# Kernel optimization log

Measured on AMD Instinct MI355X. Metric: run time of the kernel, lower is better.

The kernel has to match this reference:

```python
import jax, jax.numpy as jnp
import numpy as np

# Model hyperparameters (match init_kwargs)
G = 256      # graph_size
K = 6        # conv kernel size
CH = 8       # channels
ROWS = 4
COLS = 3
B = 64       # batch
H = G - K + 1  # conv output side (square) = 251


def setup_inputs() -> dict:
    key = jax.random.key(0)
    k1, k2, k3, k4 = jax.random.split(key, 4)
    x = jax.random.normal(k1, (B, G, G), dtype=jnp.float32)
    # Conv2d(1, CH, (K,K)) weights, kaiming_normal_ (fan_in = 1*K*K, gain=sqrt(2))
    fan_in = 1 * K * K
    conv_w = jax.random.normal(k2, (CH, 1, K, K), dtype=jnp.float32) * np.float32(np.sqrt(2.0 / fan_in))
    # torch Conv2d default bias init: U(-1/sqrt(fan_in), 1/sqrt(fan_in))
    bound = np.float32(1.0 / np.sqrt(fan_in))
    conv_b = jax.random.uniform(k3, (CH,), dtype=jnp.float32, minval=-bound, maxval=bound)
    # coef parameter [CH, ROWS, COLS], kaiming_normal_ (fan_in = ROWS*COLS)
    coef = jax.random.normal(k4, (CH, ROWS, COLS), dtype=jnp.float32) * np.float32(np.sqrt(2.0 / (ROWS * COLS)))
    return {"x": x, "conv_w": conv_w, "conv_b": conv_b, "coef": coef}


def _traces_of_powers(C):
    """C: [H,H]. Returns traces of C^(i+2) for i in 0..ROWS-1 (matches torch loop:
    x_series[0]=C@C; at step i it records trace(x_series[i]) = trace(C^(i+2))."""
    def step(P, _):
        return C @ P, jnp.trace(P)
    _, ts = jax.lax.scan(step, C @ C, None, length=ROWS)
    return ts  # [ROWS]


def reference(x, conv_w, conv_b, coef):
    # conv over each sample treated as [1,1,G,G] -> vectorized as [B,1,G,G]
    y = jax.lax.conv_general_dilated(
        x[:, None], conv_w, window_strides=(1, 1), padding='VALID',
        dimension_numbers=('NCHW', 'OIHW', 'NCHW'))
    y = y + conv_b[None, :, None, None]           # [B, CH, H, H]

    ts = jax.vmap(jax.vmap(_traces_of_powers))(y)  # [B, CH, ROWS]

    jpow = jnp.arange(1, COLS + 1, dtype=jnp.float32)            # exponents j+1
    ret = ts[..., None] ** jpow                                  # [B, CH, ROWS, COLS]
    numel = jnp.float32(H * H)
    exps = (jnp.arange(ROWS, dtype=jnp.float32)[:, None]
            + jnp.arange(COLS, dtype=jnp.float32)[None, :] + 1.0)  # i+j+1
    ret = ret / (numel ** exps)                                  # [B, CH, ROWS, COLS]

    terms = coef[None] * ret
    return terms.sum(axis=(1, 2, 3))  # [B]
```

## Files before the change

### kernel.cpp

```cpp
#include <hip/hip_runtime.h>

typedef short short8 __attribute__((ext_vector_type(8)));
typedef float f32x4 __attribute__((ext_vector_type(4)));

#define B_    64
#define CH_   8
#define NBC   512
#define MATU  65536
#define H_    251
#define PADX  76
#define LDSW  40

#define SEL_HI 0x07060302u
#define SEL_LO 0x05040100u

__device__ inline unsigned short bf16r(float f){
    unsigned u = __float_as_uint(f);
    u += 0x7fffu + ((u >> 16) & 1u);
    return (unsigned short)(u >> 16);
}
__device__ inline float bf16f(unsigned short h){ return __uint_as_float(((unsigned)h) << 16); }
__device__ inline unsigned packsplit(float v){
    unsigned short h = bf16r(v);
    unsigned short l = bf16r(v - bf16f(h));
    return (((unsigned)h) << 16) | (unsigned)l;
}
__device__ inline float unpackf(unsigned u){
    return __uint_as_float(u & 0xffff0000u) + bf16f((unsigned short)(u & 0xffffu));
}

__global__ __launch_bounds__(256) void conv_pack(const float* __restrict__ x,
                                                 const float* __restrict__ w,
                                                 const float* __restrict__ bias,
                                                 unsigned* __restrict__ Ypk,
                                                 int b_base) {
    __shared__ float xt[69 * PADX];
    __shared__ float wsm[148];

    int tid = threadIdx.x;
    int tile = blockIdx.x;
    int lb = blockIdx.y;
    int cq = blockIdx.z;
    int b = b_base + lb;
    int r0 = (tile >> 2) * 64, c0 = (tile & 3) * 64;

    if (tid < 144) wsm[tid] = w[cq * 144 + tid];
    if (tid < 4)   wsm[144 + tid] = bias[cq * 4 + tid];

    const float* xb = x + (size_t)b * 65536;
    for (int idx = tid; idx < 69 * 19; idx += 256) {
        int row = idx / 19, chq = idx - row * 19;
        int gr = r0 + row, gc = c0 + chq * 4;
        float4 v = make_float4(0.f, 0.f, 0.f, 0.f);
        if (gr < 256 && gc < 256) v = *(const float4*)(xb + gr * 256 + gc);
        *(float4*)&xt[row * PADX + chq * 4] = v;
    }
    __syncthreads();

    int tx = tid & 15, ty = tid >> 4;

    float acc[4][4][4];
    #pragma unroll
    for (int cc = 0; cc < 4; ++cc) {
        float bv = wsm[144 + cc];
        #pragma unroll
        for (int i = 0; i < 4; ++i)
            #pragma unroll
            for (int j = 0; j < 4; ++j) acc[cc][i][j] = bv;
    }

    #pragma unroll
    for (int ir = 0; ir < 9; ++ir) {
        float row[9];
        {
            const float* xr = &xt[(ty * 4 + ir) * PADX + tx * 4];
            float4 ra = *(const float4*)xr;
            float4 rb = *(const float4*)(xr + 4);
            row[0] = ra.x; row[1] = ra.y; row[2] = ra.z; row[3] = ra.w;
            row[4] = rb.x; row[5] = rb.y; row[6] = rb.z; row[7] = rb.w;
            row[8] = xr[8];
        }
        #pragma unroll
        for (int cc = 0; cc < 4; ++cc) {
            const float* wc = &wsm[cc * 36];
            #pragma unroll
            for (int i = 0; i < 4; ++i) {
                int u = ir - i;
                if (u >= 0 && u < 6) {
                    #pragma unroll
                    for (int v = 0; v < 6; ++v) {
                        float wv = wc[u * 6 + v];
                        #pragma unroll
                        for (int j = 0; j < 4; ++j) acc[cc][i][j] += row[j + v] * wv;
                    }
                }
            }
        }
    }

    #pragma unroll
    for (int cc = 0; cc < 4; ++cc) {
        int ch = cq * 4 + cc;
        unsigned pk[4][4];
        #pragma unroll
        for (int i = 0; i < 4; ++i) {
            int gr = r0 + ty * 4 + i;
            #pragma unroll
            for (int j = 0; j < 4; ++j) {
                int gc = c0 + tx * 4 + j;
                float v = (gr < H_ && gc < H_) ? acc[cc][i][j] : 0.f;
                pk[i][j] = packsplit(v);
            }
        }
        unsigned* yrow = Ypk + (size_t)(lb * 8 + ch) * MATU;
        #pragma unroll
        for (int i = 0; i < 4; ++i) {
            uint4 v = make_uint4(pk[i][0], pk[i][1], pk[i][2], pk[i][3]);
            *(uint4*)&yrow[(size_t)(r0 + ty * 4 + i) * 256 + c0 + tx * 4] = v;
        }
    }
}

template<int PHASE>
__global__ __launch_bounds__(256, 4) void gemm_mfma(const unsigned* __restrict__ Apk,
                                                    const unsigned* __restrict__ Ypk,
                                                    unsigned* __restrict__ Mpk,
                                                    double* __restrict__ pdiag,
                                                    double* __restrict__ pfull,
                                                    int bc_base, int cur) {
    __shared__ __align__(16) char smem[36864];
    __shared__ double redbuf[8];

    unsigned short* Ahi = (unsigned short*)smem;
    unsigned short* Alo = (unsigned short*)(smem + 10240);
    unsigned short* Bhi = (unsigned short*)(smem + 20480);
    unsigned short* Blo = (unsigned short*)(smem + 28672);

    int tid = threadIdx.x;

    int hw = blockIdx.x;
    int xcd = hw & 7, s = hw >> 3;
    int mpx = cur >> 3;
    int lbc = xcd * mpx + (s >> 2);
    int t4 = s & 3;
    int by = t4 >> 1, bx = t4 & 1;
    int bi = by * 128, bj = bx * 128;
    int bc = bc_base + lbc;

    const unsigned* A = Apk + (size_t)lbc * MATU;

    int wid = tid >> 6, l = tid & 63;
    int wr = wid >> 1, wc = wid & 1;
    int l15 = l & 15, lk = l >> 4;

    f32x4 acc[4][4];
    #pragma unroll
    for (int m = 0; m < 4; ++m)
        #pragma unroll
        for (int n = 0; n < 4; ++n) acc[m][n] = (f32x4){0.f, 0.f, 0.f, 0.f};

    const int cl  = tid & 31;
    const int grp = tid >> 5;
    const int kq  = grp * 4;
    const int kb  = grp >> 1;
    const int koff = (grp & 1) * 4;

    for (int k0 = 0; k0 < 256; k0 += 32) {
        #pragma unroll
        for (int p = 0; p < 4; ++p) {
            int g = p * 256 + tid;
            int row = g >> 3, chn = g & 7;
            uint4 qa = *(const uint4*)(A + (size_t)(bi + row) * 256 + k0 + chn * 4);
            uint2 hv, lv;
            hv.x = __builtin_amdgcn_perm(qa.y, qa.x, SEL_HI);
            hv.y = __builtin_amdgcn_perm(qa.w, qa.z, SEL_HI);
            lv.x = __builtin_amdgcn_perm(qa.y, qa.x, SEL_LO);
            lv.y = __builtin_amdgcn_perm(qa.w, qa.z, SEL_LO);
            *(uint2*)&Ahi[row * LDSW + chn * 4] = hv;
            *(uint2*)&Alo[row * LDSW + chn * 4] = lv;
        }
        {
            const unsigned* Bp = A + (size_t)(k0 + kq) * 256 + bj + cl;
            unsigned d[4][4];
            #pragma unroll
            for (int i = 0; i < 4; ++i)
                #pragma unroll
                for (int j = 0; j < 4; ++j)
                    d[i][j] = Bp[i * 256 + j * 32];
            #pragma unroll
            for (int j = 0; j < 4; ++j) {
                int c = cl + 32 * j;
                uint2 hv, lv;
                hv.x = __builtin_amdgcn_perm(d[1][j], d[0][j], SEL_HI);
                hv.y = __builtin_amdgcn_perm(d[3][j], d[2][j], SEL_HI);
                lv.x = __builtin_amdgcn_perm(d[1][j], d[0][j], SEL_LO);
                lv.y = __builtin_amdgcn_perm(d[3][j], d[2][j], SEL_LO);
                *(uint2*)&Bhi[kb * 1024 + c * 8 + koff] = hv;
                *(uint2*)&Blo[kb * 1024 + c * 8 + koff] = lv;
            }
        }
        __syncthreads();

        short8 ah[4], al[4], bh[4], bl[4];
        #pragma unroll
        for (int m = 0; m < 4; ++m) {
            int r = wr * 64 + m * 16 + l15;
            ah[m] = *(const short8*)&Ahi[r * LDSW + lk * 8];
            al[m] = *(const short8*)&Alo[r * LDSW + lk * 8];
        }
        #pragma unroll
        for (int n = 0; n < 4; ++n) {
            int c = wc * 64 + n * 16 + l15;
            bh[n] = *(const short8*)&Bhi[lk * 1024 + c * 8];
            bl[n] = *(const short8*)&Blo[lk * 1024 + c * 8];
        }
        #pragma unroll
        for (int m = 0; m < 4; ++m)
            #pragma unroll
            for (int n = 0; n < 4; ++n) {
                acc[m][n] = __builtin_amdgcn_mfma_f32_16x16x32_bf16(ah[m], bh[n], acc[m][n], 0, 0, 0);
                acc[m][n] = __builtin_amdgcn_mfma_f32_16x16x32_bf16(ah[m], bl[n], acc[m][n], 0, 0, 0);
                acc[m][n] = __builtin_amdgcn_mfma_f32_16x16x32_bf16(al[m], bh[n], acc[m][n], 0, 0, 0);
            }
        __syncthreads();
    }

    const unsigned* Yb = Ypk + (size_t)lbc * MATU;
    unsigned* Mw = (PHASE == 1) ? (Mpk + (size_t)lbc * MATU) : nullptr;
    float s_full = 0.f, s_diag = 0.f;
    #pragma unroll
    for (int m = 0; m < 4; ++m) {
        int rg0 = bi + wr * 64 + m * 16 + lk * 4;
        #pragma unroll
        for (int n = 0; n < 4; ++n) {
            int cg = bj + wc * 64 + n * 16 + l15;
            uint4 yq = *(const uint4*)(Yb + (size_t)cg * 256 + rg0);
            unsigned yu[4] = {yq.x, yq.y, yq.z, yq.w};
            f32x4 v = acc[m][n];
            #pragma unroll
            for (int reg = 0; reg < 4; ++reg) {
                float val = v[reg];
                s_full += val * unpackf(yu[reg]);
                if (rg0 + reg == cg) s_diag += val;
                if (PHASE == 1) Mw[(size_t)(rg0 + reg) * 256 + cg] = packsplit(val);
            }
        }
    }

    double df = (double)s_full, dd = (double)s_diag;
    #pragma unroll
    for (int off = 32; off > 0; off >>= 1) {
        df += __shfl_down(df, off, 64);
        dd += __shfl_down(dd, off, 64);
    }
    __syncthreads();
    if (l == 0) { redbuf[wid] = df; redbuf[4 + wid] = dd; }
    __syncthreads();
    if (tid == 0) {
        pfull[(size_t)bc * 4 + by * 2 + bx] =
            redbuf[0] + redbuf[1] + redbuf[2] + redbuf[3];
        if (bx == by)
            pdiag[(size_t)bc * 2 + bx] =
                redbuf[4] + redbuf[5] + redbuf[6] + redbuf[7];
    }
}

__global__ void combine(const double* __restrict__ p2, const double* __restrict__ p3,
                        const double* __restrict__ p4, const double* __restrict__ p5,
                        const float* __restrict__ coef, float* __restrict__ out) {
    int b = threadIdx.x;
    if (b >= B_) return;
    const double numel = (double)(H_ * H_);
    double acc = 0.0;
    for (int ch = 0; ch < CH_; ++ch) {
        int bc = b * CH_ + ch;
        double t[4];
        t[0] = p2[bc * 2] + p2[bc * 2 + 1];
        t[1] = p3[bc * 4] + p3[bc * 4 + 1] + p3[bc * 4 + 2] + p3[bc * 4 + 3];
        t[2] = p4[bc * 2] + p4[bc * 2 + 1];
        t[3] = p5[bc * 4] + p5[bc * 4 + 1] + p5[bc * 4 + 2] + p5[bc * 4 + 3];
        double npow_i = numel;
        for (int i = 0; i < 4; ++i) {
            double tv = t[i];
            double p = tv, d = npow_i;
            for (int j = 0; j < 3; ++j) {
                acc += (double)coef[ch * 12 + i * 3 + j] * (p / d);
                p *= tv;
                d *= numel;
            }
            npow_i *= numel;
        }
    }
    out[b] = (float)acc;
}

extern "C" void kernel_launch(void* const* d_in, const int* in_sizes, int n_in,
                              void* d_out, int out_size, void* d_ws, size_t ws_size,
                              hipStream_t stream) {
    const float* x    = (const float*)d_in[0];
    const float* w    = (const float*)d_in[1];
    const float* bias = (const float*)d_in[2];
    const float* coef = (const float*)d_in[3];
    float* out = (float*)d_out;

    double* p2 = (double*)d_ws;
    double* p3 = p2 + NBC * 2;
    double* p4 = p3 + NBC * 4;
    double* p5 = p4 + NBC * 2;
    const size_t head = 65536;

    const size_t per_mat = (size_t)MATU * 4;
    size_t avail = (ws_size > head) ? ws_size - head : 0;
    int NC = (int)(avail / (2 * per_mat));
    NC &= ~7;
    if (NC > 256) NC = 256;
    if (NC < 8) NC = 8;

    unsigned* Ypk = (unsigned*)((char*)d_ws + head);
    unsigned* Mpk = Ypk + (size_t)NC * MATU;

    for (int bc0 = 0; bc0 < NBC; bc0 += NC) {
        int cur = NBC - bc0;
        if (cur > NC) cur = NC;
        int nb = cur / 8;
        conv_pack<<<dim3(16, nb, 2), 256, 0, stream>>>(x, w, bias, Ypk, bc0 / 8);
        gemm_mfma<1><<<cur * 4, 256, 0, stream>>>(Ypk, Ypk, Mpk, p2, p3, bc0, cur);
        gemm_mfma<2><<<cur * 4, 256, 0, stream>>>(Mpk, Ypk, nullptr, p4, p5, bc0, cur);
    }
    combine<<<1, 64, 0, stream>>>(p2, p3, p4, p5, coef, out);
}
```

Before: 227.1 us.

## Double-buffer LDS and prefetch next K-slice into registers in MFMA GEMM

After: 226.2 us. No clear change (-0.4%).

```diff
diff --git a/kernel.cpp b/kernel.cpp
--- a/kernel.cpp
+++ b/kernel.cpp
@@ -128,13 +128,8 @@
                                                     double* __restrict__ pdiag,
                                                     double* __restrict__ pfull,
                                                     int bc_base, int cur) {
-    __shared__ __align__(16) char smem[36864];
+    __shared__ __align__(16) char smem[73728];
     __shared__ double redbuf[8];
-
-    unsigned short* Ahi = (unsigned short*)smem;
-    unsigned short* Alo = (unsigned short*)(smem + 10240);
-    unsigned short* Bhi = (unsigned short*)(smem + 20480);
-    unsigned short* Blo = (unsigned short*)(smem + 28672);
 
     int tid = threadIdx.x;
 
@@ -165,40 +160,68 @@
     const int kb  = grp >> 1;
     const int koff = (grp & 1) * 4;
 
-    for (int k0 = 0; k0 < 256; k0 += 32) {
+    uint4 qa[4];
+    unsigned d[4][4];
+    #pragma unroll
+    for (int p = 0; p < 4; ++p) {
+        int g = p * 256 + tid;
+        qa[p] = *(const uint4*)(A + (size_t)(bi + (g >> 3)) * 256 + (g & 7) * 4);
+    }
+    {
+        const unsigned* Bp = A + (size_t)kq * 256 + bj + cl;
+        #pragma unroll
+        for (int i = 0; i < 4; ++i)
+            #pragma unroll
+            for (int j = 0; j < 4; ++j)
+                d[i][j] = Bp[i * 256 + j * 32];
+    }
+
+    for (int ks = 0; ks < 8; ++ks) {
+        char* sb = smem + (ks & 1) * 36864;
+        unsigned short* Ahi = (unsigned short*)sb;
+        unsigned short* Alo = (unsigned short*)(sb + 10240);
+        unsigned short* Bhi = (unsigned short*)(sb + 20480);
+        unsigned short* Blo = (unsigned short*)(sb + 28672);
+
         #pragma unroll
         for (int p = 0; p < 4; ++p) {
             int g = p * 256 + tid;
             int row = g >> 3, chn = g & 7;
-            uint4 qa = *(const uint4*)(A + (size_t)(bi + row) * 256 + k0 + chn * 4);
             uint2 hv, lv;
-            hv.x = __builtin_amdgcn_perm(qa.y, qa.x, SEL_HI);
-            hv.y = __builtin_amdgcn_perm(qa.w, qa.z, SEL_HI);
-            lv.x = __builtin_amdgcn_perm(qa.y, qa.x, SEL_LO);
-            lv.y = __builtin_amdgcn_perm(qa.w, qa.z, SEL_LO);
+            hv.x = __builtin_amdgcn_perm(qa[p].y, qa[p].x, SEL_HI);
+            hv.y = __builtin_amdgcn_perm(qa[p].w, qa[p].z, SEL_HI);
+            lv.x = __builtin_amdgcn_perm(qa[p].y, qa[p].x, SEL_LO);
+            lv.y = __builtin_amdgcn_perm(qa[p].w, qa[p].z, SEL_LO);
             *(uint2*)&Ahi[row * LDSW + chn * 4] = hv;
             *(uint2*)&Alo[row * LDSW + chn * 4] = lv;
         }
-        {
-            const unsigned* Bp = A + (size_t)(k0 + kq) * 256 + bj + cl;
-            unsigned d[4][4];
+        #pragma unroll
+        for (int j = 0; j < 4; ++j) {
+            int c = cl + 32 * j;
+            uint2 hv, lv;
+            hv.x = __builtin_amdgcn_perm(d[1][j], d[0][j], SEL_HI);
+            hv.y = __builtin_amdgcn_perm(d[3][j], d[2][j], SEL_HI);
+            lv.x = __builtin_amdgcn_perm(d[1][j], d[0][j], SEL_LO);
+            lv.y = __builtin_amdgcn_perm(d[3][j], d[2][j], SEL_LO);
+            *(uint2*)&Bhi[kb * 1024 + c * 8 + koff] = hv;
+            *(uint2*)&Blo[kb * 1024 + c * 8 + koff] = lv;
+        }
+
+        if (ks < 7) {
+            int k1 = (ks + 1) * 32;
+            #pragma unroll
+            for (int p = 0; p < 4; ++p) {
+                int g = p * 256 + tid;
+                qa[p] = *(const uint4*)(A + (size_t)(bi + (g >> 3)) * 256 + k1 + (g & 7) * 4);
+            }
+            const unsigned* Bp = A + (size_t)(k1 + kq) * 256 + bj + cl;
             #pragma unroll
             for (int i = 0; i < 4; ++i)
                 #pragma unroll
                 for (int j = 0; j < 4; ++j)
                     d[i][j] = Bp[i * 256 + j * 32];
-            #pragma unroll
-            for (int j = 0; j < 4; ++j) {
-                int c = cl + 32 * j;
-                uint2 hv, lv;
-                hv.x = __builtin_amdgcn_perm(d[1][j], d[0][j], SEL_HI);
-                hv.y = __builtin_amdgcn_perm(d[3][j], d[2][j], SEL_HI);
-                lv.x = __builtin_amdgcn_perm(d[1][j], d[0][j], SEL_LO);
-                lv.y = __builtin_amdgcn_perm(d[3][j], d[2][j], SEL_LO);
-                *(uint2*)&Bhi[kb * 1024 + c * 8 + koff] = hv;
-                *(uint2*)&Blo[kb * 1024 + c * 8 + koff] = lv;
-            }
-        }
+        }
+
         __syncthreads();
 
         short8 ah[4], al[4], bh[4], bl[4];
@@ -222,7 +245,6 @@
                 acc[m][n] = __builtin_amdgcn_mfma_f32_16x16x32_bf16(ah[m], bl[n], acc[m][n], 0, 0, 0);
                 acc[m][n] = __builtin_amdgcn_mfma_f32_16x16x32_bf16(al[m], bh[n], acc[m][n], 0, 0, 0);
             }
-        __syncthreads();
     }
 
     const unsigned* Yb = Ypk + (size_t)lbc * MATU;
```
